# Performance work log

Measured on AMD Instinct MI355X. Metric: run time of the kernel, lower is better.

The kernel has to match this reference:

```python
import jax, jax.numpy as jnp
import numpy as np

N = 24000      # total nodes (8000 per node type)
IN_DIM = 128
OUT_DIM = 128
H = 8          # heads
DK = 16        # out_dim // n_heads
T = 3          # node types (hard-coded in edge_attention)
R = 34         # relations (etypes 0..33 per the etype->ntype rules)
EPR = 10000    # edges per relation (DGL applies edge fn per etype)


def _rel_node_types(num_rel):
    # src/dst node type per relation, transcribed from edge_attention
    src_nt = np.array([0 if r <= 9 else (1 if r <= 21 else 2) for r in range(num_rel)], np.int32)
    def _dnt(r):
        if r <= 2 or 10 <= r <= 13 or 22 <= r <= 24:
            return 0
        if 3 <= r <= 6 or 14 <= r <= 17 or 25 <= r <= 28:
            return 1
        return 2
    dst_nt = np.array([_dnt(r) for r in range(num_rel)], np.int32)
    return src_nt, dst_nt

SRC_NT, DST_NT = _rel_node_types(R)


def setup_inputs() -> dict:
    rng = np.random.default_rng(0)
    Nt = N // T  # nodes of type t live in [t*Nt, (t+1)*Nt)
    src = np.stack([rng.integers(SRC_NT[r] * Nt, (SRC_NT[r] + 1) * Nt, EPR) for r in range(R)]).astype(np.int32)
    dst = np.stack([rng.integers(DST_NT[r] * Nt, (DST_NT[r] + 1) * Nt, EPR) for r in range(R)]).astype(np.int32)
    ks = jax.random.split(jax.random.key(0), 10)
    lin = 1.0 / np.sqrt(IN_DIM)
    return {
        'x': jax.random.normal(ks[0], (N, IN_DIM), jnp.float32),
        'src': jnp.asarray(src),
        'dst': jnp.asarray(dst),
        'Wk': jax.random.normal(ks[1], (T, IN_DIM, OUT_DIM), jnp.float32) * lin,
        'bk': jnp.zeros((T, OUT_DIM), jnp.float32),
        'Wq': jax.random.normal(ks[2], (T, IN_DIM, OUT_DIM), jnp.float32) * lin,
        'bq': jnp.zeros((T, OUT_DIM), jnp.float32),
        'Wv': jax.random.normal(ks[3], (T, IN_DIM, OUT_DIM), jnp.float32) * lin,
        'bv': jnp.zeros((T, OUT_DIM), jnp.float32),
        'Wa': jax.random.normal(ks[4], (T, OUT_DIM, OUT_DIM), jnp.float32) * lin,
        'ba': jnp.zeros((T, OUT_DIM), jnp.float32),
        'rel_att': jax.random.normal(ks[5], (R, H, DK, DK), jnp.float32) / np.sqrt(DK),
        'rel_msg': jax.random.normal(ks[6], (R, H, DK, DK), jnp.float32) / np.sqrt(DK),
        'rel_pri': jnp.ones((R, H), jnp.float32),
        'nta': jnp.ones((T,), jnp.float32),
        'nta1': jnp.ones((T,), jnp.float32),
        'skip': jnp.ones((T,), jnp.float32),
        'weight': jnp.ones((1,), jnp.float32),
        'attn_w': jax.random.normal(ks[7], (2 * DK,), jnp.float32) * 0.1,
    }


def reference(x, src, dst, Wk, bk, Wq, bq, Wv, bv, Wa, ba, rel_att, rel_msg, rel_pri, nta, nta1, skip, weight, attn_w):
    ntype = jnp.repeat(jnp.arange(T), N // T)  # node type per node id
    ridx = jnp.arange(N)

    def typed_lin(h, W, b):
        # per-node-type Linear: compute all T projections, select by node type
        return (jnp.einsum('ni,tio->tno', h, W) + b[:, None, :])[ntype, ridx]

    k = typed_lin(x, Wk, bk).reshape(N, H, DK)
    q = typed_lin(x, Wq, bq).reshape(N, H, DK)
    v = typed_lin(x, Wv, bv).reshape(N, H, DK)

    k_src = k[src]                                   # [R, Epr, H, DK]
    q_dst = q[dst]                                   # [R, Epr, H, DK]
    key_t = jnp.einsum('rehd,rhdf->rehf', k_src, rel_att)
    a = (q_dst * key_t).sum(-1) * rel_pri[:, None, :] / np.sqrt(DK)   # [R, Epr, H]
    val = jnp.einsum('rehd,rhdf->rehf', v[src], rel_msg)              # [R, Epr, H, DK]

    # GAT-style concat attention: attn_fc(cat(att_dst*q, att_src*k)) split into two dots
    wq, wk = attn_w[:DK], attn_w[DK:]
    na = jax.nn.leaky_relu(nta1[DST_NT][:, None, None] * (q_dst @ wq)
                           + nta[SRC_NT][:, None, None] * (k_src @ wk))  # [R, Epr, H]

    beta = jax.nn.sigmoid(weight[0])
    s = (a + beta * na).reshape(R * EPR, H)

    # per-(relation, dst-node) segment softmax (DGL mailbox softmax per etype)
    seg = (jnp.arange(R)[:, None] * N + dst).reshape(-1)
    m = jax.ops.segment_max(s, seg, num_segments=R * N)
    e = jnp.exp(s - m[seg])
    den = jax.ops.segment_sum(e, seg, num_segments=R * N)
    att = e / den[seg]

    vf = val.reshape(R * EPR, H, DK)
    h = jax.ops.segment_sum(att[:, :, None] * vf, seg, num_segments=R * N).reshape(R, N, OUT_DIM)

    # cross_reducer='mean': average over relations that delivered messages to a node
    cnt = jax.ops.segment_sum(jnp.ones((R * EPR,), x.dtype), seg, num_segments=R * N).reshape(R, N)
    nrel = jnp.maximum((cnt > 0).astype(x.dtype).sum(0), 1.0)
    t = h.sum(0) / nrel[:, None]                      # [N, OUT_DIM]

    trans = (jnp.einsum('no,top->tnp', t, Wa) + ba[:, None, :])[ntype, ridx]
    alpha = jax.nn.sigmoid(skip)[ntype][:, None]
    return trans * alpha + x * (1.0 - alpha)
```

## Files before the change

### kernel.cpp

```cpp
#include <hip/hip_runtime.h>

#define NN   24000
#define NTP  8000
#define HH   8
#define DKK  16
#define RR   34
#define EPRN 10000
#define NE   (RR*EPRN)
#define NB   (RR*NTP)
#define CAP  16

typedef short short8 __attribute__((ext_vector_type(8)));
typedef float f32x4  __attribute__((ext_vector_type(4)));

__device__ __forceinline__ int src_nt(int r){ return r<=9?0:(r<=21?1:2); }
__device__ __forceinline__ int dst_nt(int r){
    if (r<=2)  return 0;
    if (r<=6)  return 1;
    if (r<=9)  return 2;
    if (r<=13) return 0;
    if (r<=17) return 1;
    if (r<=21) return 2;
    if (r<=24) return 0;
    if (r<=28) return 1;
    return 2;
}

__device__ __forceinline__ unsigned short bf16rne(float a){
    unsigned int u = __float_as_uint(a);
    u += 0x7fffu + ((u >> 16) & 1u);
    return (unsigned short)(u >> 16);
}
__device__ __forceinline__ unsigned int bf2pack(float a, float b){
    unsigned int ua = __float_as_uint(a);
    unsigned int ub = __float_as_uint(b);
    ua += 0x7fffu + ((ua >> 16) & 1u);
    ub += 0x7fffu + ((ub >> 16) & 1u);
    return (ua >> 16) | (ub & 0xffff0000u);
}
__device__ __forceinline__ void unpack8(uint4 u, float* o){
    o[0] = __uint_as_float(u.x << 16); o[1] = __uint_as_float(u.x & 0xffff0000u);
    o[2] = __uint_as_float(u.y << 16); o[3] = __uint_as_float(u.y & 0xffff0000u);
    o[4] = __uint_as_float(u.z << 16); o[5] = __uint_as_float(u.z & 0xffff0000u);
    o[6] = __uint_as_float(u.w << 16); o[7] = __uint_as_float(u.w & 0xffff0000u);
}

__global__ __launch_bounds__(256) void prep_kernel(
    const float* __restrict__ Wk, const float* __restrict__ Wq,
    const float* __restrict__ Wv, const float* __restrict__ Wa,
    int* __restrict__ counts, unsigned short* __restrict__ wfrag)
{
    const int gid = blockIdx.x * 256 + threadIdx.x;
    if (gid < NB) counts[gid] = 0;
    if (blockIdx.x < 96) {
        const int tile = blockIdx.x * 4 + (threadIdx.x >> 6);
        const int lane = threadIdx.x & 63;
        const float* W;
        int s, n;
        if (tile < 288) {
            s = tile & 3;
            n = (tile >> 2) & 7;
            const int mat = (tile >> 5) % 3;
            const int tau = tile / 96;
            W = (mat == 0 ? Wk : (mat == 1 ? Wq : Wv)) + (size_t)tau * 16384;
        } else {
            const int t2 = tile - 288;
            s = t2 & 3;
            n = (t2 >> 2) & 7;
            const int tau = t2 >> 5;
            W = Wa + (size_t)tau * 16384;
        }
        const int k0  = s * 32 + (lane >> 4) * 8;
        const int col = n * 16 + (lane & 15);
        unsigned short* dstp = wfrag + (size_t)tile * 512 + lane * 8;
        #pragma unroll
        for (int i = 0; i < 8; i++)
            dstp[i] = bf16rne(W[(size_t)(k0 + i) * 128 + col]);
    }
}

__global__ __launch_bounds__(256) void qkv_mfma(
    const float* __restrict__ x,
    const float* __restrict__ bk, const float* __restrict__ bq,
    const float* __restrict__ bv,
    const unsigned short* __restrict__ wfrag,
    float* __restrict__ qo, unsigned short* __restrict__ kvb)
{
    __shared__ float qs[4][16][132];
    __shared__ unsigned short ksh[4][16][264];
    const int rb   = blockIdx.x * 64;
    const int tau  = rb / NTP;
    const int w    = threadIdx.x >> 6;
    const int lane = threadIdx.x & 63;
    const int m    = lane & 15;
    const int quad = lane >> 4;

    short8 af[4];
    {
        const float* xrow = x + (size_t)(rb + w * 16 + m) * 128;
        #pragma unroll
        for (int s = 0; s < 4; s++) {
            float4 f0 = *(const float4*)(xrow + s * 32 + quad * 8);
            float4 f1 = *(const float4*)(xrow + s * 32 + quad * 8 + 4);
            union { unsigned int u[4]; short8 v; } pk;
            pk.u[0] = bf2pack(f0.x, f0.y); pk.u[1] = bf2pack(f0.z, f0.w);
            pk.u[2] = bf2pack(f1.x, f1.y); pk.u[3] = bf2pack(f1.z, f1.w);
            af[s] = pk.v;
        }
    }

    #pragma unroll
    for (int mat = 0; mat < 3; mat++) {
        const float* bias = (mat == 0 ? bk : (mat == 1 ? bq : bv)) + tau * 128;
        #pragma unroll
        for (int n = 0; n < 8; n++) {
            float bb = bias[n * 16 + m];
            f32x4 acc = {bb, bb, bb, bb};
            #pragma unroll
            for (int s = 0; s < 4; s++) {
                const int tile = ((tau * 3 + mat) * 8 + n) * 4 + s;
                short8 bf = *(const short8*)(wfrag + (size_t)tile * 512 + lane * 8);
                acc = __builtin_amdgcn_mfma_f32_16x16x32_bf16(af[s], bf, acc, 0, 0, 0);
            }
            if (mat == 1) {
                #pragma unroll
                for (int i = 0; i < 4; i++) qs[w][quad * 4 + i][n * 16 + m] = acc[i];
            } else {
                const int off = n * 32 + (mat == 0 ? 0 : 16) + m;
                #pragma unroll
                for (int i = 0; i < 4; i++) ksh[w][quad * 4 + i][off] = bf16rne(acc[i]);
            }
        }
        if (mat == 1) {
            __syncthreads();
            #pragma unroll
            for (int j = 0; j < 8; j++) {
                const int id = lane + 64 * j;
                const int row = id >> 5, c4 = id & 31;
                float4 v = *(const float4*)(&qs[w][row][c4 * 4]);
                *(float4*)(qo + (size_t)(rb + w * 16 + row) * 128 + c4 * 4) = v;
            }
        }
    }
    __syncthreads();
    #pragma unroll
    for (int j = 0; j < 8; j++) {
        const int id = lane + 64 * j;
        const int row = id >> 5, c8 = id & 31;
        uint4 u = *(const uint4*)(&ksh[w][row][c8 * 8]);
        *(uint4*)(kvb + (size_t)(rb + w * 16 + row) * 256 + c8 * 8) = u;
    }
}

__global__ __launch_bounds__(256) void scatter_fixed(
    const int* __restrict__ src, const int* __restrict__ dst,
    int* __restrict__ counts, int* __restrict__ esrc16)
{
    int e = blockIdx.x * 256 + threadIdx.x;
    if (e >= NE) return;
    int r = e / EPRN;
    int b = r * NTP + (dst[e] - dst_nt(r) * NTP);
    int pos = atomicAdd(&counts[b], 1);
    if (pos < CAP) esrc16[(size_t)b * CAP + pos] = src[e];
}

__global__ __launch_bounds__(256) void edge_fused(
    const float* __restrict__ q, const unsigned short* __restrict__ kvb,
    const int* __restrict__ esrc16, const int* __restrict__ counts,
    const float* __restrict__ rel_att, const float* __restrict__ rel_msg,
    const float* __restrict__ rel_pri,
    const float* __restrict__ nta, const float* __restrict__ nta1,
    const float* __restrict__ weightp, const float* __restrict__ attn_w,
    unsigned short* __restrict__ t_bf)
{
    const int tid  = threadIdx.x;
    const int h    = __builtin_amdgcn_readfirstlane((tid >> 6) + 4 * blockIdx.y);
    const int dn   = blockIdx.x * 64 + (tid & 63);
    const int dtau = __builtin_amdgcn_readfirstlane(dn / NTP);
    const int dl   = dn - dtau * NTP;

    float q16[16];
    {
        const float4* qp = (const float4*)(q + (size_t)dn * 128 + h * 16);
        #pragma unroll
        for (int i = 0; i < 4; i++) ((float4*)q16)[i] = qp[i];
    }
    float qwq = 0.f;
    #pragma unroll
    for (int f = 0; f < 16; f++) qwq += q16[f] * attn_w[f];
    const float c1   = nta1[dtau];
    const float beta = 1.f / (1.f + expf(-weightp[0]));

    float th[16] = {};
    int nrel = 0;

    for (int r = 0; r < RR; r++) {
        if (dst_nt(r) != dtau) continue;
        const int b   = r * NTP + dl;
        const int beg = b * CAP;
        int cnt = counts[b];
        cnt = cnt < CAP ? cnt : CAP;
        if (!__any(cnt > 0)) continue;

        const float* Ah = rel_att + (((size_t)r * HH + h) << 8);
        float Aq[16];
        #pragma unroll
        for (int d = 0; d < 16; d++) {
            float s = 0.f;
            #pragma unroll
            for (int f = 0; f < 16; f++) s += Ah[d * 16 + f] * q16[f];
            Aq[d] = s;
        }

        const float pri = rel_pri[r * HH + h] * 0.25f;
        const float c0  = nta[src_nt(r)];

        int4 e0 = *(const int4*)(esrc16 + beg);
        int4 e1 = *(const int4*)(esrc16 + beg + 4);
        int4 e2 = make_int4(0,0,0,0), e3 = make_int4(0,0,0,0);
        if (__any(cnt > 8)) {
            e2 = *(const int4*)(esrc16 + beg + 8);
            e3 = *(const int4*)(esrc16 + beg + 12);
        }

        float den = 0.f;
        float macc[16] = {};
        #pragma unroll
        for (int ch = 0; ch < 4; ch++) {
            if (!__any(ch * 4 < cnt)) break;
            const int4 cc = (ch == 0) ? e0 : (ch == 1) ? e1 : (ch == 2) ? e2 : e3;
            #pragma unroll
            for (int t = 0; t < 4; t++) {
                const int j = ch * 4 + t;
                if (j < cnt) {
                    const int sn = (t == 0) ? cc.x : (t == 1) ? cc.y : (t == 2) ? cc.z : cc.w;
                    const uint4* kp = (const uint4*)(kvb + (size_t)sn * 256 + h * 32);
                    uint4 u0 = kp[0], u1 = kp[1], u2 = kp[2], u3 = kp[3];
                    float kk[16], vv[16];
                    unpack8(u0, kk); unpack8(u1, kk + 8);
                    unpack8(u2, vv); unpack8(u3, vv + 8);
                    float a = 0.f, kwk = 0.f;
                    #pragma unroll
                    for (int d = 0; d < 16; d++) { a += kk[d] * Aq[d]; kwk += kk[d] * attn_w[16 + d]; }
                    float nax = c1 * qwq + c0 * kwk;
                    float na  = nax >= 0.f ? nax : 0.01f * nax;
                    float es  = expf(a * pri + beta * na);
                    den += es;
                    #pragma unroll
                    for (int f = 0; f < 16; f++) macc[f] += es * vv[f];
                }
            }
        }

        if (cnt > 0) {
            nrel++;
            const float inv = 1.f / den;
            const float* Mh = rel_msg + (((size_t)r * HH + h) << 8);
            #pragma unroll
            for (int d = 0; d < 16; d++) {
                float md = macc[d] * inv;
                #pragma unroll
                for (int f = 0; f < 16; f++) th[f] += md * Mh[d * 16 + f];
            }
        }
    }

    const float innv = 1.f / (float)(nrel > 1 ? nrel : 1);
    unsigned short* op = t_bf + (size_t)dn * 128 + h * 16;
    uint4 u0, u1;
    u0.x = bf2pack(th[0] * innv,  th[1] * innv);
    u0.y = bf2pack(th[2] * innv,  th[3] * innv);
    u0.z = bf2pack(th[4] * innv,  th[5] * innv);
    u0.w = bf2pack(th[6] * innv,  th[7] * innv);
    u1.x = bf2pack(th[8] * innv,  th[9] * innv);
    u1.y = bf2pack(th[10] * innv, th[11] * innv);
    u1.z = bf2pack(th[12] * innv, th[13] * innv);
    u1.w = bf2pack(th[14] * innv, th[15] * innv);
    *(uint4*)(op)     = u0;
    *(uint4*)(op + 8) = u1;
}

__global__ __launch_bounds__(256) void final_mfma(
    const unsigned short* __restrict__ t_bf,
    const unsigned short* __restrict__ wfrag,
    const float* __restrict__ ba, const float* __restrict__ skip,
    const float* __restrict__ x, float* __restrict__ out)
{
    const int rb   = blockIdx.x * 64;
    const int tau  = rb / NTP;
    const int w    = threadIdx.x >> 6;
    const int lane = threadIdx.x & 63;
    const int m    = lane & 15;
    const int quad = lane >> 4;

    short8 af[4];
    {
        const unsigned short* trow = t_bf + (size_t)(rb + w * 16 + m) * 128;
        #pragma unroll
        for (int s = 0; s < 4; s++)
            af[s] = *(const short8*)(trow + s * 32 + quad * 8);
    }
    const float alpha = 1.f / (1.f + expf(-skip[tau]));
    const float oma   = 1.f - alpha;

    #pragma unroll
    for (int n = 0; n < 8; n++) {
        float bb = ba[tau * 128 + n * 16 + m];
        f32x4 acc = {bb, bb, bb, bb};
        #pragma unroll
        for (int s = 0; s < 4; s++) {
            const int tile = 288 + tau * 32 + n * 4 + s;
            short8 bf = *(const short8*)(wfrag + (size_t)tile * 512 + lane * 8);
            acc = __builtin_amdgcn_mfma_f32_16x16x32_bf16(af[s], bf, acc, 0, 0, 0);
        }
        #pragma unroll
        for (int i = 0; i < 4; i++) {
            const size_t idx = (size_t)(rb + w * 16 + quad * 4 + i) * 128 + n * 16 + m;
            out[idx] = acc[i] * alpha + x[idx] * oma;
        }
    }
}

extern "C" void kernel_launch(void* const* d_in, const int* in_sizes, int n_in,
                              void* d_out, int out_size, void* d_ws, size_t ws_size,
                              hipStream_t stream) {
    const float* x       = (const float*)d_in[0];
    const int*   src     = (const int*)  d_in[1];
    const int*   dst     = (const int*)  d_in[2];
    const float* Wk      = (const float*)d_in[3];
    const float* bk      = (const float*)d_in[4];
    const float* Wq      = (const float*)d_in[5];
    const float* bq      = (const float*)d_in[6];
    const float* Wv      = (const float*)d_in[7];
    const float* bv      = (const float*)d_in[8];
    const float* Wa      = (const float*)d_in[9];
    const float* ba      = (const float*)d_in[10];
    const float* rel_att = (const float*)d_in[11];
    const float* rel_msg = (const float*)d_in[12];
    const float* rel_pri = (const float*)d_in[13];
    const float* nta     = (const float*)d_in[14];
    const float* nta1    = (const float*)d_in[15];
    const float* skip    = (const float*)d_in[16];
    const float* weight  = (const float*)d_in[17];
    const float* attn_w  = (const float*)d_in[18];
    float* out = (float*)d_out;

    float* ws    = (float*)d_ws;
    float* q     = ws;
    unsigned short* kvb = (unsigned short*)(q + (size_t)NN * 128);
    unsigned short* t_bf = kvb + (size_t)NN * 256;
    int* counts  = (int*)(t_bf + (size_t)NN * 128);
    int* esrc16  = counts + NB;
    unsigned short* wfrag = (unsigned short*)(esrc16 + (size_t)NB * CAP);

    prep_kernel<<<1063, 256, 0, stream>>>(Wk, Wq, Wv, Wa, counts, wfrag);
    qkv_mfma<<<NN / 64, 256, 0, stream>>>(x, bk, bq, bv, wfrag, q, kvb);
    scatter_fixed<<<(NE + 255) / 256, 256, 0, stream>>>(src, dst, counts, esrc16);
    edge_fused<<<dim3(NN / 64, 2), 256, 0, stream>>>(
        q, kvb, esrc16, counts, rel_att, rel_msg, rel_pri,
        nta, nta1, weight, attn_w, t_bf);
    final_mfma<<<NN / 64, 256, 0, stream>>>(t_bf, wfrag, ba, skip, x, out);
}
```

Measured before the change: 235.9 us.

## Merge QKV and edge scatter kernels, store K/V as fp16, coalesce output

The QKV projection and the edge scatter are fused into one launch, with extra blocks doing the scatter, which removes one kernel launch and lets the two independent jobs overlap. K/V are now stored as fp16 instead of bf16, and the edge loop uses packed fdot2 for the key dot products when that builtin is available. The final kernel stages results in shared memory so it can do float4 coalesced reads of x and writes of out. The fp16 storage and fp16 dot products change numeric precision and could overflow for large values.

Result: faster. 217.4 us (-7.8%).

```diff
diff --git a/kernel.cpp b/kernel.cpp
--- a/kernel.cpp
+++ b/kernel.cpp
@@ -9,9 +9,20 @@
 #define NE   (RR*EPRN)
 #define NB   (RR*NTP)
 #define CAP  16
+#define NSCAT ((NE+255)/256)
 
 typedef short short8 __attribute__((ext_vector_type(8)));
 typedef float f32x4  __attribute__((ext_vector_type(4)));
+typedef _Float16 h2v __attribute__((ext_vector_type(2)));
+
+#if defined(__has_builtin)
+# if __has_builtin(__builtin_amdgcn_fdot2)
+#  define USE_FDOT2 1
+# endif
+#endif
+#ifndef USE_FDOT2
+# define USE_FDOT2 0
+#endif
 
 __device__ __forceinline__ int src_nt(int r){ return r<=9?0:(r<=21?1:2); }
 __device__ __forceinline__ int dst_nt(int r){
@@ -38,11 +49,9 @@
     ub += 0x7fffu + ((ub >> 16) & 1u);
     return (ua >> 16) | (ub & 0xffff0000u);
 }
-__device__ __forceinline__ void unpack8(uint4 u, float* o){
-    o[0] = __uint_as_float(u.x << 16); o[1] = __uint_as_float(u.x & 0xffff0000u);
-    o[2] = __uint_as_float(u.y << 16); o[3] = __uint_as_float(u.y & 0xffff0000u);
-    o[4] = __uint_as_float(u.z << 16); o[5] = __uint_as_float(u.z & 0xffff0000u);
-    o[6] = __uint_as_float(u.w << 16); o[7] = __uint_as_float(u.w & 0xffff0000u);
+__device__ __forceinline__ unsigned short f16bits(float a){
+    _Float16 h = (_Float16)a;
+    return __builtin_bit_cast(unsigned short, h);
 }
 
 __global__ __launch_bounds__(256) void prep_kernel(
@@ -79,15 +88,29 @@
     }
 }
 
-__global__ __launch_bounds__(256) void qkv_mfma(
+__global__ __launch_bounds__(256) void work1(
     const float* __restrict__ x,
     const float* __restrict__ bk, const float* __restrict__ bq,
     const float* __restrict__ bv,
     const unsigned short* __restrict__ wfrag,
-    float* __restrict__ qo, unsigned short* __restrict__ kvb)
+    const int* __restrict__ src, const int* __restrict__ dst,
+    int* __restrict__ counts, int* __restrict__ esrc16,
+    float* __restrict__ qo, unsigned short* __restrict__ kvh)
 {
     __shared__ float qs[4][16][132];
     __shared__ unsigned short ksh[4][16][264];
+
+    if (blockIdx.x >= 375) {
+        int e = (blockIdx.x - 375) * 256 + threadIdx.x;
+        if (e < NE) {
+            int r = e / EPRN;
+            int b = r * NTP + (dst[e] - dst_nt(r) * NTP);
+            int pos = atomicAdd(&counts[b], 1);
+            if (pos < CAP) esrc16[(size_t)b * CAP + pos] = src[e];
+        }
+        return;
+    }
+
     const int rb   = blockIdx.x * 64;
     const int tau  = rb / NTP;
     const int w    = threadIdx.x >> 6;
@@ -128,7 +151,7 @@
             } else {
                 const int off = n * 32 + (mat == 0 ? 0 : 16) + m;
                 #pragma unroll
-                for (int i = 0; i < 4; i++) ksh[w][quad * 4 + i][off] = bf16rne(acc[i]);
+                for (int i = 0; i < 4; i++) ksh[w][quad * 4 + i][off] = f16bits(acc[i]);
             }
         }
         if (mat == 1) {
@@ -148,24 +171,12 @@
         const int id = lane + 64 * j;
         const int row = id >> 5, c8 = id & 31;
         uint4 u = *(const uint4*)(&ksh[w][row][c8 * 8]);
-        *(uint4*)(kvb + (size_t)(rb + w * 16 + row) * 256 + c8 * 8) = u;
-    }
-}
-
-__global__ __launch_bounds__(256) void scatter_fixed(
-    const int* __restrict__ src, const int* __restrict__ dst,
-    int* __restrict__ counts, int* __restrict__ esrc16)
-{
-    int e = blockIdx.x * 256 + threadIdx.x;
-    if (e >= NE) return;
-    int r = e / EPRN;
-    int b = r * NTP + (dst[e] - dst_nt(r) * NTP);
-    int pos = atomicAdd(&counts[b], 1);
-    if (pos < CAP) esrc16[(size_t)b * CAP + pos] = src[e];
+        *(uint4*)(kvh + (size_t)(rb + w * 16 + row) * 256 + c8 * 8) = u;
+    }
 }
 
 __global__ __launch_bounds__(256) void edge_fused(
-    const float* __restrict__ q, const unsigned short* __restrict__ kvb,
+    const float* __restrict__ q, const unsigned short* __restrict__ kvh,
     const int* __restrict__ esrc16, const int* __restrict__ counts,
     const float* __restrict__ rel_att, const float* __restrict__ rel_msg,
     const float* __restrict__ rel_pri,
@@ -188,6 +199,18 @@
     float qwq = 0.f;
     #pragma unroll
     for (int f = 0; f < 16; f++) qwq += q16[f] * attn_w[f];
+#if USE_FDOT2
+    h2v aw2h[8];
+    #pragma unroll
+    for (int i = 0; i < 8; i++) {
+        h2v t; t[0] = (_Float16)attn_w[16 + 2*i]; t[1] = (_Float16)attn_w[16 + 2*i + 1];
+        aw2h[i] = t;
+    }
+#else
+    float aw2[16];
+    #pragma unroll
+    for (int f = 0; f < 16; f++) aw2[f] = attn_w[16 + f];
+#endif
     const float c1   = nta1[dtau];
     const float beta = 1.f / (1.f + expf(-weightp[0]));
 
@@ -211,6 +234,14 @@
             for (int f = 0; f < 16; f++) s += Ah[d * 16 + f] * q16[f];
             Aq[d] = s;
         }
+#if USE_FDOT2
+        h2v Aqh[8];
+        #pragma unroll
+        for (int i = 0; i < 8; i++) {
+            h2v t; t[0] = (_Float16)Aq[2*i]; t[1] = (_Float16)Aq[2*i + 1];
+            Aqh[i] = t;
+        }
+#endif
 
         const float pri = rel_pri[r * HH + h] * 0.25f;
         const float c0  = nta[src_nt(r)];
@@ -234,14 +265,40 @@
                 const int j = ch * 4 + t;
                 if (j < cnt) {
                     const int sn = (t == 0) ? cc.x : (t == 1) ? cc.y : (t == 2) ? cc.z : cc.w;
-                    const uint4* kp = (const uint4*)(kvb + (size_t)sn * 256 + h * 32);
+                    const uint4* kp = (const uint4*)(kvh + (size_t)sn * 256 + h * 32);
                     uint4 u0 = kp[0], u1 = kp[1], u2 = kp[2], u3 = kp[3];
-                    float kk[16], vv[16];
-                    unpack8(u0, kk); unpack8(u1, kk + 8);
-                    unpack8(u2, vv); unpack8(u3, vv + 8);
                     float a = 0.f, kwk = 0.f;
-                    #pragma unroll
-                    for (int d = 0; d < 16; d++) { a += kk[d] * Aq[d]; kwk += kk[d] * attn_w[16 + d]; }
+#if USE_FDOT2
+                    {
+                        const unsigned int kw[8] = {u0.x,u0.y,u0.z,u0.w,u1.x,u1.y,u1.z,u1.w};
+                        #pragma unroll
+                        for (int i = 0; i < 8; i++) {
+                            h2v kk2 = __builtin_bit_cast(h2v, kw[i]);
+                            a   = __builtin_amdgcn_fdot2(kk2, Aqh[i],  a,   false);
+                            kwk = __builtin_amdgcn_fdot2(kk2, aw2h[i], kwk, false);
+                        }
+                    }
+#else
+                    {
+                        const unsigned int kw[8] = {u0.x,u0.y,u0.z,u0.w,u1.x,u1.y,u1.z,u1.w};
+                        #pragma unroll
+                        for (int i = 0; i < 8; i++) {
+                            h2v kk2 = __builtin_bit_cast(h2v, kw[i]);
+                            float k0f = (float)kk2[0], k1f = (float)kk2[1];
+                            a   += k0f * Aq[2*i]  + k1f * Aq[2*i + 1];
+                            kwk += k0f * aw2[2*i] + k1f * aw2[2*i + 1];
+                        }
+                    }
+#endif
+                    float vv[16];
+                    {
+                        const unsigned int vw[8] = {u2.x,u2.y,u2.z,u2.w,u3.x,u3.y,u3.z,u3.w};
+                        #pragma unroll
+                        for (int i = 0; i < 8; i++) {
+                            h2v v2 = __builtin_bit_cast(h2v, vw[i]);
+                            vv[2*i] = (float)v2[0]; vv[2*i + 1] = (float)v2[1];
+                        }
+                    }
                     float nax = c1 * qwq + c0 * kwk;
                     float na  = nax >= 0.f ? nax : 0.01f * nax;
                     float es  = expf(a * pri + beta * na);
@@ -286,6 +343,7 @@
     const float* __restrict__ ba, const float* __restrict__ skip,
     const float* __restrict__ x, float* __restrict__ out)
 {
+    __shared__ float os[4][16][132];
     const int rb   = blockIdx.x * 64;
     const int tau  = rb / NTP;
     const int w    = threadIdx.x >> 6;
@@ -300,8 +358,6 @@
         for (int s = 0; s < 4; s++)
             af[s] = *(const short8*)(trow + s * 32 + quad * 8);
     }
-    const float alpha = 1.f / (1.f + expf(-skip[tau]));
-    const float oma   = 1.f - alpha;
 
     #pragma unroll
     for (int n = 0; n < 8; n++) {
@@ -314,10 +370,24 @@
             acc = __builtin_amdgcn_mfma_f32_16x16x32_bf16(af[s], bf, acc, 0, 0, 0);
         }
         #pragma unroll
-        for (int i = 0; i < 4; i++) {
-            const size_t idx = (size_t)(rb + w * 16 + quad * 4 + i) * 128 + n * 16 + m;
-            out[idx] = acc[i] * alpha + x[idx] * oma;
-        }
+        for (int i = 0; i < 4; i++) os[w][quad * 4 + i][n * 16 + m] = acc[i];
+    }
+    __syncthreads();
+    const float alpha = 1.f / (1.f + expf(-skip[tau]));
+    const float oma   = 1.f - alpha;
+    #pragma unroll
+    for (int j = 0; j < 8; j++) {
+        const int id = lane + 64 * j;
+        const int row = id >> 5, c4 = id & 31;
+        float4 t  = *(const float4*)(&os[w][row][c4 * 4]);
+        const size_t base = (size_t)(rb + w * 16 + row) * 128 + c4 * 4;
+        float4 xv = *(const float4*)(x + base);
+        float4 o;
+        o.x = t.x * alpha + xv.x * oma;
+        o.y = t.y * alpha + xv.y * oma;
+        o.z = t.z * alpha + xv.z * oma;
+        o.w = t.w * alpha + xv.w * oma;
+        *(float4*)(out + base) = o;
     }
 }
 
@@ -347,17 +417,17 @@
 
     float* ws    = (float*)d_ws;
     float* q     = ws;
-    unsigned short* kvb = (unsigned short*)(q + (size_t)NN * 128);
-    unsigned short* t_bf = kvb + (size_t)NN * 256;
+    unsigned short* kvh = (unsigned short*)(q + (size_t)NN * 128);
+    unsigned short* t_bf = kvh + (size_t)NN * 256;
     int* counts  = (int*)(t_bf + (size_t)NN * 128);
     int* esrc16  = counts + NB;
     unsigned short* wfrag = (unsigned short*)(esrc16 + (size_t)NB * CAP);
 
     prep_kernel<<<1063, 256, 0, stream>>>(Wk, Wq, Wv, Wa, counts, wfrag);
-    qkv_mfma<<<NN / 64, 256, 0, stream>>>(x, bk, bq, bv, wfrag, q, kvb);
-    scatter_fixed<<<(NE + 255) / 256, 256, 0, stream>>>(src, dst, counts, esrc16);
+    work1<<<375 + NSCAT, 256, 0, stream>>>(x, bk, bq, bv, wfrag,
+                                           src, dst, counts, esrc16, q, kvh);
     edge_fused<<<dim3(NN / 64, 2), 256, 0, stream>>>(
-        q, kvb, esrc16, counts, rel_att, rel_msg, rel_pri,
+        q, kvh, esrc16, counts, rel_att, rel_msg, rel_pri,
         nta, nta1, weight, attn_w, t_bf);
     final_mfma<<<NN / 64, 256, 0, stream>>>(t_bf, wfrag, ba, skip, x, out);
 }
```
